# Performance work log

Measured on AMD Instinct MI355X. Metric: run time of the kernel, lower is better.

The kernel has to match this reference:

```python
import jax, jax.numpy as jnp
import numpy as np

B, D, E, H, T = 16384, 1024, 8, 512, 256
NUM_TASKS = 3  # purchase, quality, price


def setup_inputs() -> dict:
    key = jax.random.key(0)
    ks = jax.random.split(key, 12)
    s_in = 1.0 / np.sqrt(D)
    s_h = 1.0 / np.sqrt(H)
    s_t = 1.0 / np.sqrt(T)
    return {
        "x": jax.random.normal(ks[0], (B, D), dtype=jnp.float32),
        # expert layer 1: [E, D, H], layer 2: [E, H, H]
        "We1": jax.random.uniform(ks[1], (E, D, H), jnp.float32, -s_in, s_in),
        "be1": jax.random.uniform(ks[2], (E, H), jnp.float32, -s_in, s_in),
        "We2": jax.random.uniform(ks[3], (E, H, H), jnp.float32, -s_h, s_h),
        "be2": jax.random.uniform(ks[4], (E, H), jnp.float32, -s_h, s_h),
        # gates (one per task): [T_tasks, D, E]
        "Wg": jax.random.uniform(ks[5], (NUM_TASKS, D, E), jnp.float32, -s_in, s_in),
        "bg": jax.random.uniform(ks[6], (NUM_TASKS, E), jnp.float32, -s_in, s_in),
        # towers: [T_tasks, H, T] then [T_tasks, T, 1]
        "Wt1": jax.random.uniform(ks[7], (NUM_TASKS, H, T), jnp.float32, -s_h, s_h),
        "bt1": jax.random.uniform(ks[8], (NUM_TASKS, T), jnp.float32, -s_h, s_h),
        "Wt2": jax.random.uniform(ks[9], (NUM_TASKS, T, 1), jnp.float32, -s_t, s_t),
        "bt2": jax.random.uniform(ks[10], (NUM_TASKS, 1), jnp.float32, -s_t, s_t),
    }


def reference(x, We1, be1, We2, be2, Wg, bg, Wt1, bt1, Wt2, bt2):
    # Batched expert MLPs (dropout = identity in eval): [B, E, H]
    h1 = jax.nn.relu(jnp.einsum("bd,edh->beh", x, We1) + be1)
    expert_out = jax.nn.relu(jnp.einsum("beh,ehk->bek", h1, We2) + be2)
    # Per-task softmax gates: [T, B, E]
    gates = jax.nn.softmax(jnp.einsum("bd,tde->tbe", x, Wg) + bg[:, None, :], axis=-1)
    # Weighted combine: [T, B, H]
    task_in = jnp.einsum("tbe,beh->tbh", gates, expert_out)
    # Towers: [T, B, 1]
    th = jax.nn.relu(jnp.einsum("tbh,thk->tbk", task_in, Wt1) + bt1[:, None, :])
    preds = jax.nn.sigmoid(jnp.einsum("tbk,tko->tbo", th, Wt2) + bt2[:, None, :])
    return (preds[0], preds[1], preds[2])
```

## Files before the change

### kernel.cpp

```cpp
#include <hip/hip_runtime.h>


#define BM 128
#define BN 128
#define BK 64

typedef __attribute__((ext_vector_type(8))) short short8;
typedef __attribute__((ext_vector_type(4))) float floatx4;
typedef __attribute__((ext_vector_type(4))) unsigned short ushortx4;
typedef __attribute__((ext_vector_type(8))) unsigned short ushortx8;

__device__ __forceinline__ unsigned short f32_to_bf16(float f) {
  unsigned int u = __float_as_uint(f);
  u += 0x7fffu + ((u >> 16) & 1u);
  return (unsigned short)(u >> 16);
}
__device__ __forceinline__ float bf16_to_f32(unsigned short h) {
  return __uint_as_float(((unsigned int)h) << 16);
}

__device__ __forceinline__ void async_cp16(const void* g, void* lds) {
  __builtin_amdgcn_global_load_lds(
      (const __attribute__((address_space(1))) void*)g,
      (__attribute__((address_space(3))) void*)lds, 16, 0, 0);
}

__device__ __forceinline__ void transpose_slice(
    const float* __restrict__ in, unsigned short* __restrict__ out,
    int K, int N, float (*tile)[33]) {
  int n0 = blockIdx.x * 32, k0 = blockIdx.y * 32;
  for (int i = threadIdx.y; i < 32; i += 8)
    tile[i][threadIdx.x] = in[(size_t)(k0 + i) * N + n0 + threadIdx.x];
  __syncthreads();
  for (int i = threadIdx.y; i < 32; i += 8)
    out[(size_t)(n0 + i) * K + k0 + threadIdx.x] = f32_to_bf16(tile[threadIdx.x][i]);
}

__global__ void prep_kernel(const float* __restrict__ We1, const float* __restrict__ We2,
                            const float* __restrict__ Wt1, const float* __restrict__ Wg,
                            unsigned short* __restrict__ W1T, unsigned short* __restrict__ W2T,
                            unsigned short* __restrict__ Wt1T, float* __restrict__ WgT) {
  __shared__ float tile[32][33];
  int z = blockIdx.z;
  if (z < 8) {
    transpose_slice(We1 + (size_t)z * 524288, W1T + (size_t)z * 524288, 1024, 512, tile);
  } else if (z < 16) {
    if (blockIdx.y < 16)
      transpose_slice(We2 + (size_t)(z - 8) * 262144, W2T + (size_t)(z - 8) * 262144, 512, 512, tile);
  } else if (z < 19) {
    if (blockIdx.x < 8 && blockIdx.y < 16)
      transpose_slice(Wt1 + (size_t)(z - 16) * 131072, Wt1T + (size_t)(z - 16) * 131072, 512, 256, tile);
  } else {
    if (blockIdx.x < 16 && blockIdx.y < 6) {
      int idx = (blockIdx.y * 16 + blockIdx.x) * 256 + threadIdx.y * 32 + threadIdx.x;
      int t = idx >> 13, r = idx & 8191, e = r >> 10, d = r & 1023;
      WgT[idx] = Wg[t * 8192 + d * 8 + e];
    }
  }
}

__global__ __launch_bounds__(256) void gates_cvt_kernel(
    const float* __restrict__ x, const float* __restrict__ WgT,
    const float* __restrict__ bg, float* __restrict__ gout,
    unsigned short* __restrict__ xb) {
  int wave = threadIdx.x >> 6, lane = threadIdx.x & 63;
  int b = blockIdx.x * 4 + wave;
  const float* xr = x + (size_t)b * 1024;
  float xv[16];
#pragma unroll
  for (int j = 0; j < 16; j++) xv[j] = xr[lane + 64 * j];
  unsigned short* xbr = xb + (size_t)b * 1024;
#pragma unroll
  for (int j = 0; j < 16; j++) xbr[lane + 64 * j] = f32_to_bf16(xv[j]);
  float mylogit = 0.f;
#pragma unroll
  for (int te = 0; te < 24; te++) {
    const float* w = WgT + te * 1024;
    float a = 0.f;
#pragma unroll
    for (int j = 0; j < 16; j++) a += xv[j] * w[lane + 64 * j];
#pragma unroll
    for (int off = 32; off > 0; off >>= 1) a += __shfl_xor(a, off, 64);
    if (lane == te) mylogit = a;
  }
  if (lane < 24) {
    int t = lane >> 3, e = lane & 7;
    float logit = mylogit + bg[lane];
    float m = logit;
    m = fmaxf(m, __shfl_xor(m, 4, 64));
    m = fmaxf(m, __shfl_xor(m, 2, 64));
    m = fmaxf(m, __shfl_xor(m, 1, 64));
    float ex = __expf(logit - m);
    float s = ex;
    s += __shfl_xor(s, 4, 64);
    s += __shfl_xor(s, 2, 64);
    s += __shfl_xor(s, 1, 64);
    gout[(size_t)t * 131072 + (size_t)b * 8 + e] = ex / s;
  }
}

__global__ __launch_bounds__(256) void gemm_bt_relu(
    const unsigned short* __restrict__ Abase, long aOffZ, int lda,
    const unsigned short* __restrict__ Bbase, long bOffZ,
    const float* __restrict__ biasBase, int biasOffZ,
    unsigned short* __restrict__ Cbase, long cOffZ, int ldc,
    int K) {
  __shared__ __align__(16) unsigned short As[BM * BK];
  __shared__ __align__(16) unsigned short Bs[BN * BK];
  const int tid = threadIdx.x;
  const int z = blockIdx.z;
  const unsigned short* A = Abase + (size_t)aOffZ * z + (size_t)blockIdx.x * BM * lda;
  const unsigned short* Bt = Bbase + (size_t)bOffZ * z + (size_t)blockIdx.y * BN * K;
  const float* bias = biasBase + (size_t)biasOffZ * z + blockIdx.y * BN;
  unsigned short* C = Cbase + (size_t)cOffZ * z + (size_t)blockIdx.x * BM * ldc + blockIdx.y * BN;

  const int wave = tid >> 6, lane = tid & 63;
  const int wm = (wave >> 1) * 64, wn = (wave & 1) * 64;
  const int lm = lane & 15, lq = lane >> 4;
  const int sw = lm & 7;

  floatx4 acc[4][4] = {};

  const int sr = tid >> 3;
  const int sc = (((tid & 7) ^ (sr & 7)) << 3);

  for (int kt = 0; kt < K; kt += BK) {
#pragma unroll
    for (int i = 0; i < 4; i++)
      async_cp16(A + (size_t)(sr + 32 * i) * lda + kt + sc,
                 (char*)As + i * 4096 + tid * 16);
#pragma unroll
    for (int i = 0; i < 4; i++)
      async_cp16(Bt + (size_t)(sr + 32 * i) * K + kt + sc,
                 (char*)Bs + i * 4096 + tid * 16);
    __syncthreads();
#pragma unroll
    for (int ks = 0; ks < 2; ks++) {
      short8 af[4], bf[4];
      const int ch = ((ks * 4 + lq) ^ sw) << 3;
#pragma unroll
      for (int i = 0; i < 4; i++)
        af[i] = *(const short8*)(As + (wm + 16 * i + lm) * BK + ch);
#pragma unroll
      for (int j = 0; j < 4; j++)
        bf[j] = *(const short8*)(Bs + (wn + 16 * j + lm) * BK + ch);
#pragma unroll
      for (int i = 0; i < 4; i++)
#pragma unroll
        for (int j = 0; j < 4; j++)
          acc[i][j] = __builtin_amdgcn_mfma_f32_16x16x32_bf16(af[i], bf[j], acc[i][j], 0, 0, 0);
    }
    __syncthreads();
  }

#pragma unroll
  for (int i = 0; i < 4; i++) {
    const int row = wm + 16 * i + lq * 4;
#pragma unroll
    for (int j = 0; j < 4; j++) {
      const int col = wn + 16 * j + lm;
      const float bv = bias[col];
#pragma unroll
      for (int v = 0; v < 4; v++) {
        float val = fmaxf(acc[i][j][v] + bv, 0.0f);
        C[(size_t)(row + v) * ldc + col] = f32_to_bf16(val);
      }
    }
  }
}


#define STAGE_A256(buf, half, tt) do {                                       \
    const int kt_ = ((tt) < NT ? (tt) : 0) << 6;                             \
    _Pragma("unroll") for (int g_ = 0; g_ < 2; ++g_) {                       \
      const int rb_ = ((half) + 2 * g_) * 64;                                \
      async_cp16(A + (size_t)(rb_ + sr) * lda + kt_ + sc,                    \
                 (char*)As + (buf) * 32768 + rb_ * 128 + tid * 16);          \
    } } while (0)

#define STAGE_B256(buf, half, tt) do {                                       \
    const int kt_ = ((tt) < NT ? (tt) : 0) << 6;                             \
    _Pragma("unroll") for (int g_ = 0; g_ < 2; ++g_) {                       \
      const int rb_ = (half) * 128 + g_ * 64;                                \
      async_cp16(Bt + (size_t)(rb_ + sr) * K + kt_ + sc,                     \
                 (char*)Bs + (buf) * 32768 + rb_ * 128 + tid * 16);          \
    } } while (0)

#define DS_A256(mi, ks)                                                      \
  (*(const short8*)(As + cur * 16384 + (wm + 16 * (mi) + lm) * 64 +          \
                    ((((ks) * 4 + lq) ^ sw) << 3)))
#define DS_B256(nj, ks)                                                      \
  (*(const short8*)(Bs + cur * 16384 + (wn + 16 * (nj) + lm) * 64 +          \
                    ((((ks) * 4 + lq) ^ sw) << 3)))

#define PHASE256(p, STAGE_STMT, ENDWAIT) do {                                \
    short8 af[2][2];                                                         \
    af[0][0] = DS_A256(2 * (p) + 0, 0); af[0][1] = DS_A256(2 * (p) + 0, 1);  \
    af[1][0] = DS_A256(2 * (p) + 1, 0); af[1][1] = DS_A256(2 * (p) + 1, 1);  \
    if ((p) == 0) {                                                          \
      _Pragma("unroll") for (int nj = 0; nj < 4; ++nj) {                     \
        bf[nj][0] = DS_B256(nj, 0); bf[nj][1] = DS_B256(nj, 1);              \
      }                                                                      \
    }                                                                        \
    STAGE_STMT;                                                              \
    __builtin_amdgcn_s_barrier();                                            \
    asm volatile("s_waitcnt lgkmcnt(0)" ::: "memory");                       \
    __builtin_amdgcn_sched_barrier(0);                                       \
    __builtin_amdgcn_s_setprio(1);                                           \
    _Pragma("unroll") for (int d_ = 0; d_ < 2; ++d_)                         \
      _Pragma("unroll") for (int nj = 0; nj < 4; ++nj)                       \
        _Pragma("unroll") for (int ks = 0; ks < 2; ++ks)                     \
          acc[2 * (p) + d_][nj] = __builtin_amdgcn_mfma_f32_16x16x32_bf16(   \
              af[d_][ks], bf[nj][ks], acc[2 * (p) + d_][nj], 0, 0, 0);       \
    __builtin_amdgcn_s_setprio(0);                                           \
    if (ENDWAIT) asm volatile("s_waitcnt vmcnt(6)" ::: "memory");            \
    __builtin_amdgcn_s_barrier();                                            \
  } while (0)

__global__ __launch_bounds__(512) void gemm256_bt_relu(
    const unsigned short* __restrict__ Abase, long aOffZ, int lda,
    const unsigned short* __restrict__ Bbase, long bOffZ,
    const float* __restrict__ biasBase, int biasOffZ,
    unsigned short* __restrict__ Cbase, long cOffZ, int ldc,
    int K) {
  __shared__ __align__(16) unsigned short As[2 * 256 * 64];
  __shared__ __align__(16) unsigned short Bs[2 * 256 * 64];
  const int tid = threadIdx.x;
  const int z = blockIdx.z;
  const unsigned short* A = Abase + (size_t)aOffZ * z + (size_t)blockIdx.x * 256 * lda;
  const unsigned short* Bt = Bbase + (size_t)bOffZ * z + (size_t)blockIdx.y * 256 * K;
  const float* bias = biasBase + (size_t)biasOffZ * z + blockIdx.y * 256;
  unsigned short* C = Cbase + (size_t)cOffZ * z + (size_t)blockIdx.x * 256 * ldc + blockIdx.y * 256;

  const int wave = tid >> 6, lane = tid & 63;
  const int wm = (wave >> 2) * 128, wn = (wave & 3) * 64;
  const int lm = lane & 15, lq = lane >> 4;
  const int sw = lm & 7;
  const int sr = tid >> 3;
  const int sc = (((tid & 7) ^ (sr & 7)) << 3);
  const int NT = K >> 6;

  floatx4 acc[8][4] = {};
  short8 bf[4][2];

  STAGE_A256(0, 0, 0); STAGE_A256(0, 1, 0); STAGE_B256(0, 0, 0); STAGE_B256(0, 1, 0);
  asm volatile("s_waitcnt vmcnt(4)" ::: "memory");
  STAGE_B256(1, 0, 1); STAGE_A256(1, 0, 1); STAGE_B256(1, 1, 1);
  asm volatile("s_waitcnt vmcnt(6)" ::: "memory");
  __builtin_amdgcn_s_barrier();

  for (int t = 0; t < NT; ++t) {
    const int cur = t & 1;
    PHASE256(0, STAGE_A256(cur ^ 1, 1, t + 1), 0);
    PHASE256(1, STAGE_B256(cur, 0, t + 2), 0);
    PHASE256(2, STAGE_A256(cur, 0, t + 2), 0);
    PHASE256(3, STAGE_B256(cur, 1, t + 2), 1);
  }

  asm volatile("s_waitcnt vmcnt(0)" ::: "memory");

  float bv[4];
#pragma unroll
  for (int nj = 0; nj < 4; ++nj) bv[nj] = bias[wn + 16 * nj + lm];
#pragma unroll
  for (int mi = 0; mi < 8; ++mi) {
    const int row = wm + 16 * mi + lq * 4;
#pragma unroll
    for (int nj = 0; nj < 4; ++nj) {
      const int col = wn + 16 * nj + lm;
#pragma unroll
      for (int v = 0; v < 4; ++v) {
        float val = fmaxf(acc[mi][nj][v] + bv[nj], 0.0f);
        C[(size_t)(row + v) * ldc + col] = f32_to_bf16(val);
      }
    }
  }
}

__global__ void combine_kernel(const unsigned short* __restrict__ eo,
                               const float* __restrict__ gates,
                               unsigned short* __restrict__ ti,
                               int b0, int Bc) {
  int tid = blockIdx.x * 256 + threadIdx.x;
  int bl = tid >> 6;
  int hc = (tid & 63) << 3;
  float g[3][8];
#pragma unroll
  for (int t = 0; t < 3; t++) {
    const floatx4* gp = (const floatx4*)(gates + ((size_t)t * 16384 + b0 + bl) * 8);
    floatx4 g0 = gp[0], g1 = gp[1];
#pragma unroll
    for (int j = 0; j < 4; j++) { g[t][j] = g0[j]; g[t][4 + j] = g1[j]; }
  }
  float out[3][8] = {};
#pragma unroll
  for (int e = 0; e < 8; e++) {
    ushortx8 v = *(const ushortx8*)(eo + ((size_t)bl * 8 + e) * 512 + hc);
#pragma unroll
    for (int j = 0; j < 8; j++) {
      float f = bf16_to_f32(v[j]);
#pragma unroll
      for (int t = 0; t < 3; t++) out[t][j] += g[t][e] * f;
    }
  }
#pragma unroll
  for (int t = 0; t < 3; t++) {
    ushortx8 o;
#pragma unroll
    for (int j = 0; j < 8; j++) o[j] = f32_to_bf16(out[t][j]);
    *(ushortx8*)(ti + ((size_t)t * Bc + bl) * 512 + hc) = o;
  }
}

__global__ __launch_bounds__(512) void tower_fused_kernel(
    const unsigned short* __restrict__ tic, const unsigned short* __restrict__ Wt1T,
    const float* __restrict__ bt1, const float* __restrict__ Wt2,
    const float* __restrict__ bt2, float* __restrict__ out,
    int b0, int Bc) {
  __shared__ __align__(16) unsigned short As[128 * 64];
  __shared__ __align__(16) unsigned short Bs[256 * 64];
  const int tid = threadIdx.x;
  const int mtiles = Bc >> 7;
  const int t = blockIdx.x / mtiles;
  const int xbl = blockIdx.x % mtiles;
  const unsigned short* A = tic + ((size_t)t * Bc + (size_t)xbl * 128) * 512;
  const unsigned short* Bt = Wt1T + (size_t)t * 131072;

  const int wave = tid >> 6, lane = tid & 63;
  const int wm = (wave >> 2) * 64, wn = (wave & 3) * 64;
  const int lm = lane & 15, lq = lane >> 4;
  const int sw = lm & 7;

  floatx4 acc[4][4] = {};

  const int sr = tid >> 3;
  const int sc = (((tid & 7) ^ (sr & 7)) << 3);

  for (int kt = 0; kt < 512; kt += 64) {
#pragma unroll
    for (int i = 0; i < 2; i++)
      async_cp16(A + (size_t)(sr + 64 * i) * 512 + kt + sc,
                 (char*)As + i * 8192 + tid * 16);
#pragma unroll
    for (int i = 0; i < 4; i++)
      async_cp16(Bt + (size_t)(sr + 64 * i) * 512 + kt + sc,
                 (char*)Bs + i * 8192 + tid * 16);
    __syncthreads();
#pragma unroll
    for (int ks = 0; ks < 2; ks++) {
      short8 af[4], bf[4];
      const int ch = ((ks * 4 + lq) ^ sw) << 3;
#pragma unroll
      for (int i = 0; i < 4; i++)
        af[i] = *(const short8*)(As + (wm + 16 * i + lm) * 64 + ch);
#pragma unroll
      for (int j = 0; j < 4; j++)
        bf[j] = *(const short8*)(Bs + (wn + 16 * j + lm) * 64 + ch);
#pragma unroll
      for (int i = 0; i < 4; i++)
#pragma unroll
        for (int j = 0; j < 4; j++)
          acc[i][j] = __builtin_amdgcn_mfma_f32_16x16x32_bf16(af[i], bf[j], acc[i][j], 0, 0, 0);
    }
    __syncthreads();
  }

  float b1v[4], w2v[4];
#pragma unroll
  for (int j = 0; j < 4; j++) {
    int col = wn + 16 * j + lm;
    b1v[j] = bt1[t * 256 + col];
    w2v[j] = Wt2[t * 256 + col];
  }
  float* pt = (float*)As;
#pragma unroll
  for (int i = 0; i < 4; i++) {
#pragma unroll
    for (int v = 0; v < 4; v++) {
      float p = 0.f;
#pragma unroll
      for (int j = 0; j < 4; j++)
        p += fmaxf(acc[i][j][v] + b1v[j], 0.0f) * w2v[j];
      p += __shfl_xor(p, 1, 64);
      p += __shfl_xor(p, 2, 64);
      p += __shfl_xor(p, 4, 64);
      p += __shfl_xor(p, 8, 64);
      if (lm == 0) pt[(wm + 16 * i + lq * 4 + v) * 4 + (wave & 3)] = p;
    }
  }
  __syncthreads();
  if (tid < 128) {
    float s = pt[tid * 4] + pt[tid * 4 + 1] + pt[tid * 4 + 2] + pt[tid * 4 + 3] + bt2[t];
    out[(t << 14) + b0 + xbl * 128 + tid] = 1.f / (1.f + __expf(-s));
  }
}

extern "C" void kernel_launch(void* const* d_in, const int* in_sizes, int n_in,
                              void* d_out, int out_size, void* d_ws, size_t ws_size,
                              hipStream_t stream) {
  (void)in_sizes; (void)n_in; (void)out_size;
  const float* x   = (const float*)d_in[0];
  const float* We1 = (const float*)d_in[1];
  const float* be1 = (const float*)d_in[2];
  const float* We2 = (const float*)d_in[3];
  const float* be2 = (const float*)d_in[4];
  const float* Wg  = (const float*)d_in[5];
  const float* bg  = (const float*)d_in[6];
  const float* Wt1 = (const float*)d_in[7];
  const float* bt1 = (const float*)d_in[8];
  const float* Wt2 = (const float*)d_in[9];
  const float* bt2 = (const float*)d_in[10];
  float* out = (float*)d_out;

  char* ws = (char*)d_ws;
  unsigned short* xb   = (unsigned short*)(ws + 0);
  unsigned short* W1T  = (unsigned short*)(ws + 33554432);
  unsigned short* W2T  = (unsigned short*)(ws + 41943040);
  unsigned short* Wt1T = (unsigned short*)(ws + 46137344);
  float*          gts  = (float*)(ws + 46923776);
  float*          WgT  = (float*)(ws + 48496640);
  const size_t fixed = 48594944;

  size_t rem = ws_size > fixed ? ws_size - fixed : 0;
  int Bc = 16384;
  while (Bc > 512 && (size_t)Bc * 19456 > rem) Bc >>= 1;
  const int nc = 16384 / Bc;

  char* cb = ws + fixed;
  unsigned short* h1c = (unsigned short*)(cb);
  unsigned short* eoc = (unsigned short*)(cb + (size_t)Bc * 8192);
  unsigned short* tic = (unsigned short*)(cb + (size_t)Bc * 16384);

  prep_kernel<<<dim3(16, 32, 20), dim3(32, 8), 0, stream>>>(We1, We2, Wt1, Wg, W1T, W2T, Wt1T, WgT);
  gates_cvt_kernel<<<4096, 256, 0, stream>>>(x, WgT, bg, gts, xb);

  for (int c = 0; c < nc; c++) {
    const unsigned short* xbc = xb + (size_t)c * Bc * 1024;
    if (Bc >= 4096) {
      gemm256_bt_relu<<<dim3(Bc / 256, 2, 8), 512, 0, stream>>>(
          xbc, 0L, 1024, W1T, 524288L, be1, 512, h1c, 512L, 4096, 1024);
      gemm256_bt_relu<<<dim3(Bc / 256, 2, 8), 512, 0, stream>>>(
          h1c, 512L, 4096, W2T, 262144L, be2, 512, eoc, 512L, 4096, 512);
    } else {
      gemm_bt_relu<<<dim3(Bc / 128, 4, 8), 256, 0, stream>>>(
          xbc, 0L, 1024, W1T, 524288L, be1, 512, h1c, 512L, 4096, 1024);
      gemm_bt_relu<<<dim3(Bc / 128, 4, 8), 256, 0, stream>>>(
          h1c, 512L, 4096, W2T, 262144L, be2, 512, eoc, 512L, 4096, 512);
    }
    combine_kernel<<<Bc / 4, 256, 0, stream>>>(eoc, gts, tic, c * Bc, Bc);
    tower_fused_kernel<<<3 * (Bc / 128), 512, 0, stream>>>(
        tic, Wt1T, bt1, Wt2, bt2, out, c * Bc, Bc);
  }
}
```

Baseline: 520.1 us.

## Fuse gate combine into tower kernel and drop 256-tile expert GEMM

Removes the separate combine kernel and its task_in buffer. The tower kernel now reads expert outputs and gates directly, computes the weighted sum per K-tile in registers, and writes it to LDS before the tower GEMM. It also deletes the hand-pipelined 256x256 expert GEMM and always uses the 128x128 gemm_bt_relu. The smaller per-row workspace lets chunks be larger. The tradeoff is that the three task blocks each re-read the expert outputs with synchronous loads, and the expert GEMMs, which dominate runtime, lose the tuned large-tile path.

```diff
diff --git a/kernel.cpp b/kernel.cpp
--- a/kernel.cpp
+++ b/kernel.cpp
@@ -169,151 +169,9 @@
   }
 }
 
-
-#define STAGE_A256(buf, half, tt) do {                                       \
-    const int kt_ = ((tt) < NT ? (tt) : 0) << 6;                             \
-    _Pragma("unroll") for (int g_ = 0; g_ < 2; ++g_) {                       \
-      const int rb_ = ((half) + 2 * g_) * 64;                                \
-      async_cp16(A + (size_t)(rb_ + sr) * lda + kt_ + sc,                    \
-                 (char*)As + (buf) * 32768 + rb_ * 128 + tid * 16);          \
-    } } while (0)
-
-#define STAGE_B256(buf, half, tt) do {                                       \
-    const int kt_ = ((tt) < NT ? (tt) : 0) << 6;                             \
-    _Pragma("unroll") for (int g_ = 0; g_ < 2; ++g_) {                       \
-      const int rb_ = (half) * 128 + g_ * 64;                                \
-      async_cp16(Bt + (size_t)(rb_ + sr) * K + kt_ + sc,                     \
-                 (char*)Bs + (buf) * 32768 + rb_ * 128 + tid * 16);          \
-    } } while (0)
-
-#define DS_A256(mi, ks)                                                      \
-  (*(const short8*)(As + cur * 16384 + (wm + 16 * (mi) + lm) * 64 +          \
-                    ((((ks) * 4 + lq) ^ sw) << 3)))
-#define DS_B256(nj, ks)                                                      \
-  (*(const short8*)(Bs + cur * 16384 + (wn + 16 * (nj) + lm) * 64 +          \
-                    ((((ks) * 4 + lq) ^ sw) << 3)))
-
-#define PHASE256(p, STAGE_STMT, ENDWAIT) do {                                \
-    short8 af[2][2];                                                         \
-    af[0][0] = DS_A256(2 * (p) + 0, 0); af[0][1] = DS_A256(2 * (p) + 0, 1);  \
-    af[1][0] = DS_A256(2 * (p) + 1, 0); af[1][1] = DS_A256(2 * (p) + 1, 1);  \
-    if ((p) == 0) {                                                          \
-      _Pragma("unroll") for (int nj = 0; nj < 4; ++nj) {                     \
-        bf[nj][0] = DS_B256(nj, 0); bf[nj][1] = DS_B256(nj, 1);              \
-      }                                                                      \
-    }                                                                        \
-    STAGE_STMT;                                                              \
-    __builtin_amdgcn_s_barrier();                                            \
-    asm volatile("s_waitcnt lgkmcnt(0)" ::: "memory");                       \
-    __builtin_amdgcn_sched_barrier(0);                                       \
-    __builtin_amdgcn_s_setprio(1);                                           \
-    _Pragma("unroll") for (int d_ = 0; d_ < 2; ++d_)                         \
-      _Pragma("unroll") for (int nj = 0; nj < 4; ++nj)                       \
-        _Pragma("unroll") for (int ks = 0; ks < 2; ++ks)                     \
-          acc[2 * (p) + d_][nj] = __builtin_amdgcn_mfma_f32_16x16x32_bf16(   \
-              af[d_][ks], bf[nj][ks], acc[2 * (p) + d_][nj], 0, 0, 0);       \
-    __builtin_amdgcn_s_setprio(0);                                           \
-    if (ENDWAIT) asm volatile("s_waitcnt vmcnt(6)" ::: "memory");            \
-    __builtin_amdgcn_s_barrier();                                            \
-  } while (0)
-
-__global__ __launch_bounds__(512) void gemm256_bt_relu(
-    const unsigned short* __restrict__ Abase, long aOffZ, int lda,
-    const unsigned short* __restrict__ Bbase, long bOffZ,
-    const float* __restrict__ biasBase, int biasOffZ,
-    unsigned short* __restrict__ Cbase, long cOffZ, int ldc,
-    int K) {
-  __shared__ __align__(16) unsigned short As[2 * 256 * 64];
-  __shared__ __align__(16) unsigned short Bs[2 * 256 * 64];
-  const int tid = threadIdx.x;
-  const int z = blockIdx.z;
-  const unsigned short* A = Abase + (size_t)aOffZ * z + (size_t)blockIdx.x * 256 * lda;
-  const unsigned short* Bt = Bbase + (size_t)bOffZ * z + (size_t)blockIdx.y * 256 * K;
-  const float* bias = biasBase + (size_t)biasOffZ * z + blockIdx.y * 256;
-  unsigned short* C = Cbase + (size_t)cOffZ * z + (size_t)blockIdx.x * 256 * ldc + blockIdx.y * 256;
-
-  const int wave = tid >> 6, lane = tid & 63;
-  const int wm = (wave >> 2) * 128, wn = (wave & 3) * 64;
-  const int lm = lane & 15, lq = lane >> 4;
-  const int sw = lm & 7;
-  const int sr = tid >> 3;
-  const int sc = (((tid & 7) ^ (sr & 7)) << 3);
-  const int NT = K >> 6;
-
-  floatx4 acc[8][4] = {};
-  short8 bf[4][2];
-
-  STAGE_A256(0, 0, 0); STAGE_A256(0, 1, 0); STAGE_B256(0, 0, 0); STAGE_B256(0, 1, 0);
-  asm volatile("s_waitcnt vmcnt(4)" ::: "memory");
-  STAGE_B256(1, 0, 1); STAGE_A256(1, 0, 1); STAGE_B256(1, 1, 1);
-  asm volatile("s_waitcnt vmcnt(6)" ::: "memory");
-  __builtin_amdgcn_s_barrier();
-
-  for (int t = 0; t < NT; ++t) {
-    const int cur = t & 1;
-    PHASE256(0, STAGE_A256(cur ^ 1, 1, t + 1), 0);
-    PHASE256(1, STAGE_B256(cur, 0, t + 2), 0);
-    PHASE256(2, STAGE_A256(cur, 0, t + 2), 0);
-    PHASE256(3, STAGE_B256(cur, 1, t + 2), 1);
-  }
-
-  asm volatile("s_waitcnt vmcnt(0)" ::: "memory");
-
-  float bv[4];
-#pragma unroll
-  for (int nj = 0; nj < 4; ++nj) bv[nj] = bias[wn + 16 * nj + lm];
-#pragma unroll
-  for (int mi = 0; mi < 8; ++mi) {
-    const int row = wm + 16 * mi + lq * 4;
-#pragma unroll
-    for (int nj = 0; nj < 4; ++nj) {
-      const int col = wn + 16 * nj + lm;
-#pragma unroll
-      for (int v = 0; v < 4; ++v) {
-        float val = fmaxf(acc[mi][nj][v] + bv[nj], 0.0f);
-        C[(size_t)(row + v) * ldc + col] = f32_to_bf16(val);
-      }
-    }
-  }
-}
-
-__global__ void combine_kernel(const unsigned short* __restrict__ eo,
-                               const float* __restrict__ gates,
-                               unsigned short* __restrict__ ti,
-                               int b0, int Bc) {
-  int tid = blockIdx.x * 256 + threadIdx.x;
-  int bl = tid >> 6;
-  int hc = (tid & 63) << 3;
-  float g[3][8];
-#pragma unroll
-  for (int t = 0; t < 3; t++) {
-    const floatx4* gp = (const floatx4*)(gates + ((size_t)t * 16384 + b0 + bl) * 8);
-    floatx4 g0 = gp[0], g1 = gp[1];
-#pragma unroll
-    for (int j = 0; j < 4; j++) { g[t][j] = g0[j]; g[t][4 + j] = g1[j]; }
-  }
-  float out[3][8] = {};
-#pragma unroll
-  for (int e = 0; e < 8; e++) {
-    ushortx8 v = *(const ushortx8*)(eo + ((size_t)bl * 8 + e) * 512 + hc);
-#pragma unroll
-    for (int j = 0; j < 8; j++) {
-      float f = bf16_to_f32(v[j]);
-#pragma unroll
-      for (int t = 0; t < 3; t++) out[t][j] += g[t][e] * f;
-    }
-  }
-#pragma unroll
-  for (int t = 0; t < 3; t++) {
-    ushortx8 o;
-#pragma unroll
-    for (int j = 0; j < 8; j++) o[j] = f32_to_bf16(out[t][j]);
-    *(ushortx8*)(ti + ((size_t)t * Bc + bl) * 512 + hc) = o;
-  }
-}
-
 __global__ __launch_bounds__(512) void tower_fused_kernel(
-    const unsigned short* __restrict__ tic, const unsigned short* __restrict__ Wt1T,
+    const unsigned short* __restrict__ eoc, const float* __restrict__ gates,
+    const unsigned short* __restrict__ Wt1T,
     const float* __restrict__ bt1, const float* __restrict__ Wt2,
     const float* __restrict__ bt2, float* __restrict__ out,
     int b0, int Bc) {
@@ -323,7 +181,6 @@
   const int mtiles = Bc >> 7;
   const int t = blockIdx.x / mtiles;
   const int xbl = blockIdx.x % mtiles;
-  const unsigned short* A = tic + ((size_t)t * Bc + (size_t)xbl * 128) * 512;
   const unsigned short* Bt = Wt1T + (size_t)t * 131072;
 
   const int wave = tid >> 6, lane = tid & 63;
@@ -336,11 +193,33 @@
   const int sr = tid >> 3;
   const int sc = (((tid & 7) ^ (sr & 7)) << 3);
 
+  float gv[2][8];
+#pragma unroll
+  for (int r = 0; r < 2; r++) {
+    const floatx4* gp = (const floatx4*)(
+        gates + ((size_t)t * 16384 + b0 + (size_t)xbl * 128 + sr + 64 * r) * 8);
+    floatx4 g0 = gp[0], g1 = gp[1];
+#pragma unroll
+    for (int j = 0; j < 4; j++) { gv[r][j] = g0[j]; gv[r][4 + j] = g1[j]; }
+  }
+
   for (int kt = 0; kt < 512; kt += 64) {
 #pragma unroll
-    for (int i = 0; i < 2; i++)
-      async_cp16(A + (size_t)(sr + 64 * i) * 512 + kt + sc,
-                 (char*)As + i * 8192 + tid * 16);
+    for (int r = 0; r < 2; r++) {
+      const int bl = xbl * 128 + sr + 64 * r;
+      float s[8] = {};
+#pragma unroll
+      for (int e = 0; e < 8; e++) {
+        ushortx8 v = *(const ushortx8*)(eoc + ((size_t)bl * 8 + e) * 512 + kt + sc);
+        const float g = gv[r][e];
+#pragma unroll
+        for (int j = 0; j < 8; j++) s[j] += g * bf16_to_f32(v[j]);
+      }
+      ushortx8 o;
+#pragma unroll
+      for (int j = 0; j < 8; j++) o[j] = f32_to_bf16(s[j]);
+      *(ushortx8*)((char*)As + r * 8192 + tid * 16) = o;
+    }
 #pragma unroll
     for (int i = 0; i < 4; i++)
       async_cp16(Bt + (size_t)(sr + 64 * i) * 512 + kt + sc,
@@ -423,32 +302,23 @@
 
   size_t rem = ws_size > fixed ? ws_size - fixed : 0;
   int Bc = 16384;
-  while (Bc > 512 && (size_t)Bc * 19456 > rem) Bc >>= 1;
+  while (Bc > 512 && (size_t)Bc * 16384 > rem) Bc >>= 1;
   const int nc = 16384 / Bc;
 
   char* cb = ws + fixed;
   unsigned short* h1c = (unsigned short*)(cb);
   unsigned short* eoc = (unsigned short*)(cb + (size_t)Bc * 8192);
-  unsigned short* tic = (unsigned short*)(cb + (size_t)Bc * 16384);
 
   prep_kernel<<<dim3(16, 32, 20), dim3(32, 8), 0, stream>>>(We1, We2, Wt1, Wg, W1T, W2T, Wt1T, WgT);
   gates_cvt_kernel<<<4096, 256, 0, stream>>>(x, WgT, bg, gts, xb);
 
   for (int c = 0; c < nc; c++) {
     const unsigned short* xbc = xb + (size_t)c * Bc * 1024;
-    if (Bc >= 4096) {
-      gemm256_bt_relu<<<dim3(Bc / 256, 2, 8), 512, 0, stream>>>(
-          xbc, 0L, 1024, W1T, 524288L, be1, 512, h1c, 512L, 4096, 1024);
-      gemm256_bt_relu<<<dim3(Bc / 256, 2, 8), 512, 0, stream>>>(
-          h1c, 512L, 4096, W2T, 262144L, be2, 512, eoc, 512L, 4096, 512);
-    } else {
-      gemm_bt_relu<<<dim3(Bc / 128, 4, 8), 256, 0, stream>>>(
-          xbc, 0L, 1024, W1T, 524288L, be1, 512, h1c, 512L, 4096, 1024);
-      gemm_bt_relu<<<dim3(Bc / 128, 4, 8), 256, 0, stream>>>(
-          h1c, 512L, 4096, W2T, 262144L, be2, 512, eoc, 512L, 4096, 512);
-    }
-    combine_kernel<<<Bc / 4, 256, 0, stream>>>(eoc, gts, tic, c * Bc, Bc);
+    gemm_bt_relu<<<dim3(Bc / 128, 4, 8), 256, 0, stream>>>(
+        xbc, 0L, 1024, W1T, 524288L, be1, 512, h1c, 512L, 4096, 1024);
+    gemm_bt_relu<<<dim3(Bc / 128, 4, 8), 256, 0, stream>>>(
+        h1c, 512L, 4096, W2T, 262144L, be2, 512, eoc, 512L, 4096, 512);
     tower_fused_kernel<<<3 * (Bc / 128), 512, 0, stream>>>(
-        tic, Wt1T, bt1, Wt2, bt2, out, c * Bc, Bc);
-  }
-}
+        eoc, gts, Wt1T, bt1, Wt2, bt2, out, c * Bc, Bc);
+  }
+}
```

Result: no change. 525.5 us (+1.0%).
